# Optimization experiments

Hardware: AMD Instinct MI355X
Metric: run time of the kernel (lower is better)

Reference implementation:

```python
import jax, jax.numpy as jnp
import numpy as np
import math

GATE_LB_FAST = 0.0
GATE_LB_SLOW = 0.85


def fwht(x):
    # Matches torch impl: interleaved butterfly via stack of even/odd lanes.
    d = x.shape[-1]
    steps = int(round(math.log2(d)))
    for _ in range(steps):
        left = x[..., 0::2]
        right = x[..., 1::2]
        x = jnp.stack([left + right, left - right], axis=-1).reshape(x.shape)
    return x * (d ** -0.5)


def hproj(x, scales):
    # y = s4*F(s3*F(s2*F(s1*F(s0*x))))
    h = x * scales[0]
    for i in range(1, scales.shape[0]):
        h = fwht(h) * scales[i]
    return h


def gated_scan(f, v):
    # h_t = f_t*h_{t-1} + (1-f_t)*v_t over time axis 1; f,v: [B,T,D]
    def step(h, fv):
        ft, vt = fv
        h = ft * h + (1.0 - ft) * vt
        return h, h
    init = jnp.zeros((v.shape[0], v.shape[2]), dtype=v.dtype)
    _, hs = jax.lax.scan(step, init, (jnp.moveaxis(f, 1, 0), jnp.moveaxis(v, 1, 0)))
    return jnp.moveaxis(hs, 0, 1)


def setup_inputs() -> dict:
    key = jax.random.key(0)
    ks = jax.random.split(key, 9)
    B, T, D = 4, 2048, 1024
    TOT = 1024  # n_heads*d_head == d_model -> HadamardProj has no extra Linear
    return {
        "x": jax.random.normal(ks[0], (B, T, D), dtype=jnp.float32),
        "fast_gate_scales": jax.random.normal(ks[1], (5, D), dtype=jnp.float32) * 0.02,
        "fast_val_scales": jax.random.normal(ks[2], (5, D), dtype=jnp.float32) * 0.02,
        "fast_out_w": jax.random.normal(ks[3], (TOT, D), dtype=jnp.float32) * 0.02,
        "slow_gate_scales": jax.random.normal(ks[4], (5, D), dtype=jnp.float32) * 0.02,
        "slow_val_scales": jax.random.normal(ks[5], (5, D), dtype=jnp.float32) * 0.02,
        "slow_out_w": jax.random.normal(ks[6], (TOT, D), dtype=jnp.float32) * 0.02,
        "merge_w": jax.random.normal(ks[7], (D, 2 * TOT), dtype=jnp.float32) * 0.02,
        "norm_w": jnp.ones((2 * TOT,), dtype=jnp.float32),
    }


def reference(x, fast_gate_scales, fast_val_scales, fast_out_w,
              slow_gate_scales, slow_val_scales, slow_out_w, merge_w, norm_w):
    # fast stream
    f_gate = jax.nn.sigmoid(hproj(x, fast_gate_scales) + 0.5)
    f_forget = GATE_LB_FAST + (1.0 - GATE_LB_FAST) * f_gate
    f_val = hproj(x, fast_val_scales)
    fast_h = gated_scan(f_forget, f_val)
    fast_out = jax.nn.sigmoid(jnp.einsum('btd,od->bto', x, fast_out_w)) * fast_h
    # slow stream
    s_gate = jax.nn.sigmoid(hproj(x, slow_gate_scales) + 0.5)
    s_forget = GATE_LB_SLOW + (1.0 - GATE_LB_SLOW) * s_gate
    s_val = hproj(x, slow_val_scales)
    slow_h = gated_scan(s_forget, s_val)
    slow_out = jax.nn.sigmoid(jnp.einsum('btd,od->bto', x, slow_out_w)) * slow_h
    merged = jnp.concatenate([fast_out, slow_out], axis=-1)  # [B,T,2*TOT]
    normed = merged * jax.lax.rsqrt(jnp.mean(merged * merged, axis=-1, keepdims=True) + 1e-6) * norm_w
    return jnp.einsum('btm,dm->btd', normed, merge_w)
```

## Files before the change

kernel.cpp:

```cpp
#include <hip/hip_runtime.h>
#include <stdint.h>


typedef __attribute__((ext_vector_type(8))) short short8;
typedef __attribute__((ext_vector_type(4))) float f32x4;
typedef __attribute__((ext_vector_type(2))) float f32x2;
typedef __attribute__((ext_vector_type(4))) unsigned short ushort4v;
typedef __attribute__((ext_vector_type(2))) unsigned short ushort2v;

typedef const __attribute__((address_space(1))) unsigned int* as1_u32p;
typedef __attribute__((address_space(3))) unsigned int* as3_u32p;

__device__ __forceinline__ void cp16(const void* g, void* l) {
  __builtin_amdgcn_global_load_lds((as1_u32p)(uintptr_t)g,
                                   (as3_u32p)(unsigned int)(uintptr_t)l,
                                   16, 0, 0);
}

__device__ __forceinline__ float b2f(unsigned short h) {
  union { unsigned int u; float f; } v; v.u = ((unsigned int)h) << 16; return v.f;
}
__device__ __forceinline__ unsigned short f2b(float f) {
  union { float f; unsigned int u; } v; v.f = f;
  unsigned int r = v.u + 0x7fffu + ((v.u >> 16) & 1u);
  return (unsigned short)(r >> 16);
}
__device__ __forceinline__ float sigmoidf_(float z) {
  return __builtin_amdgcn_rcpf(1.0f + __expf(-z));
}

__global__ __launch_bounds__(256) void k_scanA(
    const float* __restrict__ x,
    const float* __restrict__ fgs, const float* __restrict__ fvs,
    const float* __restrict__ sgs, const float* __restrict__ svs,
    const float* __restrict__ fow, const float* __restrict__ sow,
    const float* __restrict__ mw,  const float* __restrict__ nw,
    float* __restrict__ PF, float* __restrict__ HF,
    float* __restrict__ PS, float* __restrict__ HS,
    unsigned short* __restrict__ wcat, unsigned short* __restrict__ w2,
    float* __restrict__ rowsum) {
  if (blockIdx.x >= 512) {
    int g = (blockIdx.x - 512) * 256 + threadIdx.x;
    if (g < 524288) {
      int i = g * 4;
      const float* src = (i < 1048576) ? (fow + i) : (sow + (i - 1048576));
      f32x4 v = *(const f32x4*)src;
      ushort4v o = { f2b(v.x), f2b(v.y), f2b(v.z), f2b(v.w) };
      *(ushort4v*)&wcat[i] = o;
    } else if (g < 1048576) {
      int i = (g - 524288) * 4;
      int m = i & 2047;
      f32x4 v = *(const f32x4*)&mw[i];
      f32x4 s = *(const f32x4*)&nw[m];
      ushort4v o = { f2b(v.x * s.x), f2b(v.y * s.y), f2b(v.z * s.z), f2b(v.w * s.w) };
      *(ushort4v*)&w2[i] = o;
    } else if (g < 1056768) {
      rowsum[g - 1048576] = 0.f;
    }
    return;
  }
  int g = blockIdx.x * 256 + threadIdx.x;
  int d0 = (g & 511) << 1;
  int rest = g >> 9;
  int chunk = rest & 63, b = rest >> 6;
  float fg0 = 1.f, fg1 = 1.f, fv0 = 1.f, fv1 = 1.f;
  float sg0 = 1.f, sg1 = 1.f, sv0 = 1.f, sv1 = 1.f;
#pragma unroll
  for (int i = 0; i < 5; ++i) {
    f32x2 a = *(const f32x2*)&fgs[i * 1024 + d0]; fg0 *= a.x; fg1 *= a.y;
    f32x2 bq = *(const f32x2*)&fvs[i * 1024 + d0]; fv0 *= bq.x; fv1 *= bq.y;
    f32x2 c = *(const f32x2*)&sgs[i * 1024 + d0]; sg0 *= c.x; sg1 *= c.y;
    f32x2 e = *(const f32x2*)&svs[i * 1024 + d0]; sv0 *= e.x; sv1 *= e.y;
  }
  size_t base = ((size_t)(b * 2048 + chunk * 32)) * 1024 + d0;
  float pF0 = 1.f, hF0 = 0.f, pS0 = 1.f, hS0 = 0.f;
  float pF1 = 1.f, hF1 = 0.f, pS1 = 1.f, hS1 = 0.f;
#pragma unroll 8
  for (int t = 0; t < 32; ++t) {
    f32x2 xv = *(const f32x2*)&x[base + (size_t)t * 1024];
    float fF0 = sigmoidf_(xv.x * fg0 + 0.5f);
    hF0 = fF0 * hF0 + (1.f - fF0) * (xv.x * fv0); pF0 *= fF0;
    float fS0 = 0.85f + 0.15f * sigmoidf_(xv.x * sg0 + 0.5f);
    hS0 = fS0 * hS0 + (1.f - fS0) * (xv.x * sv0); pS0 *= fS0;
    float fF1 = sigmoidf_(xv.y * fg1 + 0.5f);
    hF1 = fF1 * hF1 + (1.f - fF1) * (xv.y * fv1); pF1 *= fF1;
    float fS1 = 0.85f + 0.15f * sigmoidf_(xv.y * sg1 + 0.5f);
    hS1 = fS1 * hS1 + (1.f - fS1) * (xv.y * sv1); pS1 *= fS1;
  }
  int idx = (b * 64 + chunk) * 1024 + d0;
  *(f32x2*)&PF[idx] = f32x2{pF0, pF1};
  *(f32x2*)&HF[idx] = f32x2{hF0, hF1};
  *(f32x2*)&PS[idx] = f32x2{pS0, pS1};
  *(f32x2*)&HS[idx] = f32x2{hS0, hS1};
}

__global__ __launch_bounds__(256) void k_scanC(
    const float* __restrict__ x,
    const float* __restrict__ fgs, const float* __restrict__ fvs,
    const float* __restrict__ sgs, const float* __restrict__ svs,
    const float* __restrict__ PF, const float* __restrict__ HF,
    const float* __restrict__ PS, const float* __restrict__ HS,
    unsigned short* __restrict__ xb, unsigned short* __restrict__ hcat) {
  int g = blockIdx.x * 256 + threadIdx.x;
  int d0 = (g & 511) << 1;
  int rest = g >> 9;
  int chunk = rest & 63, b = rest >> 6;
  float fg0 = 1.f, fg1 = 1.f, fv0 = 1.f, fv1 = 1.f;
  float sg0 = 1.f, sg1 = 1.f, sv0 = 1.f, sv1 = 1.f;
#pragma unroll
  for (int i = 0; i < 5; ++i) {
    f32x2 a = *(const f32x2*)&fgs[i * 1024 + d0]; fg0 *= a.x; fg1 *= a.y;
    f32x2 bq = *(const f32x2*)&fvs[i * 1024 + d0]; fv0 *= bq.x; fv1 *= bq.y;
    f32x2 c = *(const f32x2*)&sgs[i * 1024 + d0]; sg0 *= c.x; sg1 *= c.y;
    f32x2 e = *(const f32x2*)&svs[i * 1024 + d0]; sv0 *= e.x; sv1 *= e.y;
  }
  float cF0 = 0.f, cF1 = 0.f, cS0 = 0.f, cS1 = 0.f;
  {
    int base_i = b * 64 * 1024 + d0;
    int c = 0;
    for (; c + 4 <= chunk; c += 4) {
      f32x2 pf[4], hf[4], ps[4], hs[4];
#pragma unroll
      for (int j = 0; j < 4; ++j) {
        int i = base_i + (c + j) * 1024;
        pf[j] = *(const f32x2*)&PF[i]; hf[j] = *(const f32x2*)&HF[i];
        ps[j] = *(const f32x2*)&PS[i]; hs[j] = *(const f32x2*)&HS[i];
      }
#pragma unroll
      for (int j = 0; j < 4; ++j) {
        cF0 = hf[j].x + pf[j].x * cF0; cF1 = hf[j].y + pf[j].y * cF1;
        cS0 = hs[j].x + ps[j].x * cS0; cS1 = hs[j].y + ps[j].y * cS1;
      }
    }
    for (; c < chunk; ++c) {
      int i = base_i + c * 1024;
      f32x2 pf = *(const f32x2*)&PF[i], hf = *(const f32x2*)&HF[i];
      f32x2 ps = *(const f32x2*)&PS[i], hs = *(const f32x2*)&HS[i];
      cF0 = hf.x + pf.x * cF0; cF1 = hf.y + pf.y * cF1;
      cS0 = hs.x + ps.x * cS0; cS1 = hs.y + ps.y * cS1;
    }
  }
  size_t base = ((size_t)(b * 2048 + chunk * 32)) * 1024 + d0;
  float pF0 = 1.f, hF0 = 0.f, pS0 = 1.f, hS0 = 0.f;
  float pF1 = 1.f, hF1 = 0.f, pS1 = 1.f, hS1 = 0.f;
#pragma unroll 4
  for (int t = 0; t < 32; ++t) {
    f32x2 xv = *(const f32x2*)&x[base + (size_t)t * 1024];
    *(ushort2v*)&xb[base + (size_t)t * 1024] = ushort2v{f2b(xv.x), f2b(xv.y)};
    float fF0 = sigmoidf_(xv.x * fg0 + 0.5f);
    hF0 = fF0 * hF0 + (1.f - fF0) * (xv.x * fv0); pF0 *= fF0;
    float fS0 = 0.85f + 0.15f * sigmoidf_(xv.x * sg0 + 0.5f);
    hS0 = fS0 * hS0 + (1.f - fS0) * (xv.x * sv0); pS0 *= fS0;
    float fF1 = sigmoidf_(xv.y * fg1 + 0.5f);
    hF1 = fF1 * hF1 + (1.f - fF1) * (xv.y * fv1); pF1 *= fF1;
    float fS1 = 0.85f + 0.15f * sigmoidf_(xv.y * sg1 + 0.5f);
    hS1 = fS1 * hS1 + (1.f - fS1) * (xv.y * sv1); pS1 *= fS1;
    size_t bt = (size_t)(b * 2048 + chunk * 32 + t);
    *(ushort2v*)&hcat[bt * 2048 + d0] =
        ushort2v{f2b(hF0 + pF0 * cF0), f2b(hF1 + pF1 * cF1)};
    *(ushort2v*)&hcat[bt * 2048 + 1024 + d0] =
        ushort2v{f2b(hS0 + pS0 * cS0), f2b(hS1 + pS1 * cS1)};
  }
}

template <int BT, int MODE>
__global__ __launch_bounds__(512, 2) void k_gemm8(
    const unsigned short* __restrict__ A, const unsigned short* __restrict__ B,
    const int K,
    const unsigned short* __restrict__ hcat, unsigned short* __restrict__ merged,
    float* __restrict__ rowsum, float* __restrict__ out) {
  constexpr int BN = 64 * BT;
  __shared__ __align__(16) unsigned short sA[2][256 * 64];
  __shared__ __align__(16) unsigned short sB[2][BN * 64];

  const int tid = threadIdx.x;
  const int wv = tid >> 6, ln = tid & 63;
  const int wm = wv >> 2, wn = wv & 3;
  const int fr = ln & 15, fq = ln >> 4;
  const int sl0 = (fq ^ (fr & 7)) * 8;
  const int sl1 = ((fq + 4) ^ (fr & 7)) * 8;
  const int rA = (wm * 128 + fr) * 64;
  const int rB = (wn * 16 * BT + fr) * 64;

  const int swz = (blockIdx.x & 7) * 32 + (blockIdx.x >> 3);
  const int bm = (swz >> 3) * 256;
  const int bn = (swz & 7) * BN;

  const int srow = tid >> 3, sc = tid & 7;
  const int clog = (sc ^ (srow & 7)) * 8;
  const unsigned short* pA[4]; int lofA[4];
#pragma unroll
  for (int j = 0; j < 4; ++j) {
    pA[j] = A + (size_t)(bm + j * 64 + srow) * K + clog;
    lofA[j] = (j * 64 + srow) * 64 + sc * 8;
  }
  const unsigned short* pB[BT]; int lofB[BT];
#pragma unroll
  for (int j = 0; j < BT; ++j) {
    pB[j] = B + (size_t)(bn + j * 64 + srow) * K + clog;
    lofB[j] = (j * 64 + srow) * 64 + sc * 8;
  }

  f32x4 acc[8][BT];
  const f32x4 z4 = {0.f, 0.f, 0.f, 0.f};
#pragma unroll
  for (int i = 0; i < 8; ++i)
#pragma unroll
    for (int j = 0; j < BT; ++j) acc[i][j] = z4;

  const int NT = K >> 6;
#pragma unroll
  for (int j = 0; j < 4; ++j) cp16(pA[j], &sA[0][lofA[j]]);
#pragma unroll
  for (int j = 0; j < BT; ++j) cp16(pB[j], &sB[0][lofB[j]]);
#pragma unroll
  for (int j = 0; j < BT; ++j) cp16(pB[j] + 64, &sB[1][lofB[j]]);
  if constexpr (BT == 4) asm volatile("s_waitcnt vmcnt(4)" ::: "memory");
  else                   asm volatile("s_waitcnt vmcnt(2)" ::: "memory");
  __builtin_amdgcn_s_barrier();
  __builtin_amdgcn_sched_barrier(0);

  for (int t = 0; t < NT; ++t) {
    const unsigned short* cA = &sA[t & 1][0];
    const unsigned short* cB = &sB[t & 1][0];
    unsigned short* dA = &sA[(t + 1) & 1][0];
    unsigned short* dB = &sB[t & 1][0];
    const size_t ko1 = (size_t)(t + 1) * 64;
    const size_t ko2 = (size_t)(t + 2) * 64;
    short8 aA[4], aB[4], b0[BT], b1[BT];
#pragma unroll
    for (int m = 0; m < 4; ++m) aA[m] = *(const short8*)&cA[rA + m * 1024 + sl0];
#pragma unroll
    for (int n = 0; n < BT; ++n) b0[n] = *(const short8*)&cB[rB + n * 1024 + sl0];
    if (t + 1 < NT) { cp16(pA[0] + ko1, &dA[lofA[0]]);
                      cp16(pA[1] + ko1, &dA[lofA[1]]); }
    __builtin_amdgcn_s_barrier();
    asm volatile("s_waitcnt lgkmcnt(0)" ::: "memory");
    __builtin_amdgcn_sched_barrier(0);
    __builtin_amdgcn_s_setprio(1);
#pragma unroll
    for (int m = 0; m < 4; ++m)
#pragma unroll
      for (int n = 0; n < BT; ++n)
        acc[m][n] = __builtin_amdgcn_mfma_f32_16x16x32_bf16(aA[m], b0[n], acc[m][n], 0, 0, 0);
    __builtin_amdgcn_s_setprio(0);
    __builtin_amdgcn_s_barrier();
#pragma unroll
    for (int m = 0; m < 4; ++m) aB[m] = *(const short8*)&cA[rA + (4 + m) * 1024 + sl0];
    if (t + 1 < NT) { cp16(pA[2] + ko1, &dA[lofA[2]]);
                      cp16(pA[3] + ko1, &dA[lofA[3]]); }
    __builtin_amdgcn_s_barrier();
    asm volatile("s_waitcnt lgkmcnt(0)" ::: "memory");
    __builtin_amdgcn_sched_barrier(0);
    __builtin_amdgcn_s_setprio(1);
#pragma unroll
    for (int m = 0; m < 4; ++m)
#pragma unroll
      for (int n = 0; n < BT; ++n)
        acc[4 + m][n] = __builtin_amdgcn_mfma_f32_16x16x32_bf16(aB[m], b0[n], acc[4 + m][n], 0, 0, 0);
    __builtin_amdgcn_s_setprio(0);
    __builtin_amdgcn_s_barrier();
#pragma unroll
    for (int m = 0; m < 4; ++m) aA[m] = *(const short8*)&cA[rA + m * 1024 + sl1];
#pragma unroll
    for (int n = 0; n < BT; ++n) b1[n] = *(const short8*)&cB[rB + n * 1024 + sl1];
    __builtin_amdgcn_s_barrier();
    asm volatile("s_waitcnt lgkmcnt(0)" ::: "memory");
    __builtin_amdgcn_sched_barrier(0);
    __builtin_amdgcn_s_setprio(1);
#pragma unroll
    for (int m = 0; m < 4; ++m)
#pragma unroll
      for (int n = 0; n < BT; ++n)
        acc[m][n] = __builtin_amdgcn_mfma_f32_16x16x32_bf16(aA[m], b1[n], acc[m][n], 0, 0, 0);
    __builtin_amdgcn_s_setprio(0);
    __builtin_amdgcn_s_barrier();
#pragma unroll
    for (int m = 0; m < 4; ++m) aB[m] = *(const short8*)&cA[rA + (4 + m) * 1024 + sl1];
    if (t + 2 < NT) {
#pragma unroll
      for (int j = 0; j < BT; ++j) cp16(pB[j] + ko2, &dB[lofB[j]]);
    }
    __builtin_amdgcn_s_barrier();
    asm volatile("s_waitcnt lgkmcnt(0)" ::: "memory");
    __builtin_amdgcn_sched_barrier(0);
    __builtin_amdgcn_s_setprio(1);
#pragma unroll
    for (int m = 0; m < 4; ++m)
#pragma unroll
      for (int n = 0; n < BT; ++n)
        acc[4 + m][n] = __builtin_amdgcn_mfma_f32_16x16x32_bf16(aB[m], b1[n], acc[4 + m][n], 0, 0, 0);
    __builtin_amdgcn_s_setprio(0);
    if (t < NT - 2) {
      if constexpr (BT == 4) asm volatile("s_waitcnt vmcnt(4)" ::: "memory");
      else                   asm volatile("s_waitcnt vmcnt(2)" ::: "memory");
    } else if (t == NT - 2) {
      asm volatile("s_waitcnt vmcnt(0)" ::: "memory");
    }
    __builtin_amdgcn_s_barrier();
    __builtin_amdgcn_sched_barrier(0);
  }

  const int er0 = fq * 4;
  if (MODE == 1) {
#pragma unroll
    for (int mi = 0; mi < 8; ++mi) {
#pragma unroll
      for (int r = 0; r < 4; ++r) {
        const int m = bm + wm * 128 + mi * 16 + er0 + r;
        float s = 0.f;
#pragma unroll
        for (int ni = 0; ni < BT; ++ni) {
          const int n = bn + wn * 16 * BT + ni * 16 + fr;
          const size_t idx = (size_t)m * 2048 + n;
          float v = sigmoidf_(acc[mi][ni][r]) * b2f(hcat[idx]);
          merged[idx] = f2b(v);
          s += v * v;
        }
        s += __shfl_xor(s, 1); s += __shfl_xor(s, 2);
        s += __shfl_xor(s, 4); s += __shfl_xor(s, 8);
        if (fr == 0) atomicAdd(&rowsum[m], s);
      }
    }
  } else {
#pragma unroll
    for (int mi = 0; mi < 8; ++mi) {
#pragma unroll
      for (int r = 0; r < 4; ++r) {
        const int m = bm + wm * 128 + mi * 16 + er0 + r;
        const float rf = rsqrtf(rowsum[m] * (1.0f / 2048.0f) + 1e-6f);
#pragma unroll
        for (int ni = 0; ni < BT; ++ni) {
          const int n = bn + wn * 16 * BT + ni * 16 + fr;
          out[(size_t)m * 1024 + n] = rf * acc[mi][ni][r];
        }
      }
    }
  }
}

extern "C" void kernel_launch(void* const* d_in, const int* in_sizes, int n_in,
                              void* d_out, int out_size, void* d_ws, size_t ws_size,
                              hipStream_t stream) {
  const float* x   = (const float*)d_in[0];
  const float* fgs = (const float*)d_in[1];
  const float* fvs = (const float*)d_in[2];
  const float* fow = (const float*)d_in[3];
  const float* sgs = (const float*)d_in[4];
  const float* svs = (const float*)d_in[5];
  const float* sow = (const float*)d_in[6];
  const float* mw  = (const float*)d_in[7];
  const float* nw  = (const float*)d_in[8];
  float* out = (float*)d_out;

  char* ws = (char*)d_ws;
  float* rowsum = (float*)(ws + 0);
  unsigned short* xb   = (unsigned short*)(ws + 32768);
  unsigned short* wcat = (unsigned short*)(ws + 16809984);
  unsigned short* w2   = (unsigned short*)(ws + 21004288);
  unsigned short* hcat = (unsigned short*)(ws + 25198592);
  unsigned short* mg   = (unsigned short*)(ws + 58753024);
  float* PF = (float*)(ws + 58753024);
  float* HF = (float*)(ws + 58753024 + 1 * 1048576);
  float* PS = (float*)(ws + 58753024 + 2 * 1048576);
  float* HS = (float*)(ws + 58753024 + 3 * 1048576);

  k_scanA<<<4640, 256, 0, stream>>>(x, fgs, fvs, sgs, svs, fow, sow, mw, nw,
                                    PF, HF, PS, HS, wcat, w2, rowsum);
  k_scanC<<<512, 256, 0, stream>>>(x, fgs, fvs, sgs, svs, PF, HF, PS, HS,
                                   xb, hcat);
  k_gemm8<4, 1><<<256, 512, 0, stream>>>(
      xb, wcat, 1024, hcat, mg, rowsum, nullptr);
  k_gemm8<2, 2><<<256, 512, 0, stream>>>(
      mg, w2, 2048, nullptr, nullptr, rowsum, out);
}
```

Baseline: 221.7 us.

## Prefetch A tiles two iterations ahead and hoist A fragment reads earlier

A-tile global-to-LDS copies now run two k-steps ahead, into the same buffer being consumed, instead of one step ahead into the alternate buffer. This matches the existing B-tile prefetch depth, and the prologue loads both stages of A. All A fragments for both k-halves are read from LDS early into registers, so the A buffer can be overwritten mid-iteration. The goal is to hide global load latency better, at the cost of more registers and more outstanding memory ops (vmcnt raised).

```diff
diff --git a/kernel.cpp b/kernel.cpp
--- a/kernel.cpp
+++ b/kernel.cpp
@@ -214,26 +214,25 @@
 #pragma unroll
   for (int j = 0; j < BT; ++j) cp16(pB[j], &sB[0][lofB[j]]);
 #pragma unroll
+  for (int j = 0; j < 4; ++j) cp16(pA[j] + 64, &sA[1][lofA[j]]);
+#pragma unroll
   for (int j = 0; j < BT; ++j) cp16(pB[j] + 64, &sB[1][lofB[j]]);
-  if constexpr (BT == 4) asm volatile("s_waitcnt vmcnt(4)" ::: "memory");
-  else                   asm volatile("s_waitcnt vmcnt(2)" ::: "memory");
+  if constexpr (BT == 4) asm volatile("s_waitcnt vmcnt(8)" ::: "memory");
+  else                   asm volatile("s_waitcnt vmcnt(6)" ::: "memory");
   __builtin_amdgcn_s_barrier();
   __builtin_amdgcn_sched_barrier(0);
 
   for (int t = 0; t < NT; ++t) {
     const unsigned short* cA = &sA[t & 1][0];
     const unsigned short* cB = &sB[t & 1][0];
-    unsigned short* dA = &sA[(t + 1) & 1][0];
+    unsigned short* dA = &sA[t & 1][0];
     unsigned short* dB = &sB[t & 1][0];
-    const size_t ko1 = (size_t)(t + 1) * 64;
     const size_t ko2 = (size_t)(t + 2) * 64;
-    short8 aA[4], aB[4], b0[BT], b1[BT];
-#pragma unroll
-    for (int m = 0; m < 4; ++m) aA[m] = *(const short8*)&cA[rA + m * 1024 + sl0];
+    short8 aA0[4], aB0[4], aA1[4], aB1[4], b0[BT], b1[BT];
+#pragma unroll
+    for (int m = 0; m < 4; ++m) aA0[m] = *(const short8*)&cA[rA + m * 1024 + sl0];
 #pragma unroll
     for (int n = 0; n < BT; ++n) b0[n] = *(const short8*)&cB[rB + n * 1024 + sl0];
-    if (t + 1 < NT) { cp16(pA[0] + ko1, &dA[lofA[0]]);
-                      cp16(pA[1] + ko1, &dA[lofA[1]]); }
     __builtin_amdgcn_s_barrier();
     asm volatile("s_waitcnt lgkmcnt(0)" ::: "memory");
     __builtin_amdgcn_sched_barrier(0);
@@ -242,13 +241,16 @@
     for (int m = 0; m < 4; ++m)
 #pragma unroll
       for (int n = 0; n < BT; ++n)
-        acc[m][n] = __builtin_amdgcn_mfma_f32_16x16x32_bf16(aA[m], b0[n], acc[m][n], 0, 0, 0);
+        acc[m][n] = __builtin_amdgcn_mfma_f32_16x16x32_bf16(aA0[m], b0[n], acc[m][n], 0, 0, 0);
     __builtin_amdgcn_s_setprio(0);
     __builtin_amdgcn_s_barrier();
 #pragma unroll
-    for (int m = 0; m < 4; ++m) aB[m] = *(const short8*)&cA[rA + (4 + m) * 1024 + sl0];
-    if (t + 1 < NT) { cp16(pA[2] + ko1, &dA[lofA[2]]);
-                      cp16(pA[3] + ko1, &dA[lofA[3]]); }
+    for (int m = 0; m < 4; ++m) aB0[m] = *(const short8*)&cA[rA + (4 + m) * 1024 + sl0];
+#pragma unroll
+    for (int m = 0; m < 4; ++m) aA1[m] = *(const short8*)&cA[rA + m * 1024 + sl1];
+#pragma unroll
+    for (int m = 0; m < 4; ++m) aB1[m] = *(const short8*)&cA[rA + (4 + m) * 1024 + sl1];
+    asm volatile("s_waitcnt lgkmcnt(8)" ::: "memory");
     __builtin_amdgcn_s_barrier();
     asm volatile("s_waitcnt lgkmcnt(0)" ::: "memory");
     __builtin_amdgcn_sched_barrier(0);
@@ -257,13 +259,15 @@
     for (int m = 0; m < 4; ++m)
 #pragma unroll
       for (int n = 0; n < BT; ++n)
-        acc[4 + m][n] = __builtin_amdgcn_mfma_f32_16x16x32_bf16(aB[m], b0[n], acc[4 + m][n], 0, 0, 0);
+        acc[4 + m][n] = __builtin_amdgcn_mfma_f32_16x16x32_bf16(aB0[m], b0[n], acc[4 + m][n], 0, 0, 0);
     __builtin_amdgcn_s_setprio(0);
     __builtin_amdgcn_s_barrier();
 #pragma unroll
-    for (int m = 0; m < 4; ++m) aA[m] = *(const short8*)&cA[rA + m * 1024 + sl1];
-#pragma unroll
     for (int n = 0; n < BT; ++n) b1[n] = *(const short8*)&cB[rB + n * 1024 + sl1];
+    if (t + 2 < NT) {
+#pragma unroll
+      for (int j = 0; j < 4; ++j) cp16(pA[j] + ko2, &dA[lofA[j]]);
+    }
     __builtin_amdgcn_s_barrier();
     asm volatile("s_waitcnt lgkmcnt(0)" ::: "memory");
     __builtin_amdgcn_sched_barrier(0);
@@ -272,28 +276,25 @@
     for (int m = 0; m < 4; ++m)
 #pragma unroll
       for (int n = 0; n < BT; ++n)
-        acc[m][n] = __builtin_amdgcn_mfma_f32_16x16x32_bf16(aA[m], b1[n], acc[m][n], 0, 0, 0);
+        acc[m][n] = __builtin_amdgcn_mfma_f32_16x16x32_bf16(aA1[m], b1[n], acc[m][n], 0, 0, 0);
     __builtin_amdgcn_s_setprio(0);
     __builtin_amdgcn_s_barrier();
-#pragma unroll
-    for (int m = 0; m < 4; ++m) aB[m] = *(const short8*)&cA[rA + (4 + m) * 1024 + sl1];
     if (t + 2 < NT) {
 #pragma unroll
       for (int j = 0; j < BT; ++j) cp16(pB[j] + ko2, &dB[lofB[j]]);
     }
     __builtin_amdgcn_s_barrier();
-    asm volatile("s_waitcnt lgkmcnt(0)" ::: "memory");
     __builtin_amdgcn_sched_barrier(0);
     __builtin_amdgcn_s_setprio(1);
 #pragma unroll
     for (int m = 0; m < 4; ++m)
 #pragma unroll
       for (int n = 0; n < BT; ++n)
-        acc[4 + m][n] = __builtin_amdgcn_mfma_f32_16x16x32_bf16(aB[m], b1[n], acc[4 + m][n], 0, 0, 0);
+        acc[4 + m][n] = __builtin_amdgcn_mfma_f32_16x16x32_bf16(aB1[m], b1[n], acc[4 + m][n], 0, 0, 0);
     __builtin_amdgcn_s_setprio(0);
     if (t < NT - 2) {
-      if constexpr (BT == 4) asm volatile("s_waitcnt vmcnt(4)" ::: "memory");
-      else                   asm volatile("s_waitcnt vmcnt(2)" ::: "memory");
+      if constexpr (BT == 4) asm volatile("s_waitcnt vmcnt(8)" ::: "memory");
+      else                   asm volatile("s_waitcnt vmcnt(6)" ::: "memory");
     } else if (t == NT - 2) {
       asm volatile("s_waitcnt vmcnt(0)" ::: "memory");
     }
```

Result: no change. 224.7 us (+1.4%).
